# Performance work log

Hardware: AMD Instinct MI355X
Metric: run time of the kernel (lower is better)

Reference implementation:

```python
import jax, jax.numpy as jnp
import numpy as np

EPS = 1e-5
H = 6  # num_heads

def batchnorm(x, g, b):
    # BatchNorm1d over node dim using batch statistics (biased var, eps=1e-5)
    mu = x.mean(0)
    var = jnp.mean((x - mu) ** 2, 0)
    return (x - mu) * jax.lax.rsqrt(var + EPS) * g + b

def setup_inputs() -> dict:
    key = jax.random.key(0)
    ks = jax.random.split(key, 16)
    N, E, D = 20000, 200000, 384
    DH = 2 * D  # mlp hidden = dim * mlp_ratio(2.0)
    s = 0.05
    lin = lambda k, i, o: jax.random.normal(k, (i, o), jnp.float32) * s
    inp = {}
    inp['x'] = jax.random.normal(ks[0], (N, D), jnp.float32)
    inp['edge_index'] = jax.random.randint(ks[1], (2, E), 0, N)
    inp['edge_attr'] = jax.random.normal(ks[2], (E, D), jnp.float32)
    # norm1
    inp['g1'] = jnp.ones((D,), jnp.float32); inp['b1'] = jnp.zeros((D,), jnp.float32)
    # TransformerConv-style attention (concat=True, beta=False, edge_dim=D)
    inp['Wq'] = lin(ks[3], D, D); inp['bq'] = jnp.zeros((D,), jnp.float32)
    inp['Wk'] = lin(ks[4], D, D); inp['bk'] = jnp.zeros((D,), jnp.float32)
    inp['Wv'] = lin(ks[5], D, D); inp['bv'] = jnp.zeros((D,), jnp.float32)
    inp['We'] = lin(ks[6], D, D)  # lin_edge, no bias
    inp['Wskip'] = lin(ks[7], D, D); inp['bskip'] = jnp.zeros((D,), jnp.float32)
    # norm2
    inp['g2'] = jnp.ones((D,), jnp.float32); inp['b2'] = jnp.zeros((D,), jnp.float32)
    # Mlp
    inp['W1'] = lin(ks[8], D, DH); inp['bm1'] = jnp.zeros((DH,), jnp.float32)
    inp['W2'] = lin(ks[9], DH, D); inp['bm2'] = jnp.zeros((D,), jnp.float32)
    return inp

def reference(x, edge_index, edge_attr, g1, b1, Wq, bq, Wk, bk, Wv, bv, We, Wskip, bskip, g2, b2, W1, bm1, W2, bm2):
    N, D = x.shape
    Dh = D // H
    scale = 1.0 / jnp.sqrt(jnp.float32(Dh))
    h = batchnorm(x, g1, b1)
    q = (h @ Wq + bq).reshape(N, H, Dh)
    k = (h @ Wk + bk).reshape(N, H, Dh)
    v = (h @ Wv + bv).reshape(N, H, Dh)
    e = (edge_attr @ We).reshape(-1, H, Dh)  # [E,H,Dh]
    src, dst = edge_index[0], edge_index[1]
    ke = k[src] + e  # edge attr added to key
    ve = v[src] + e  # and to value (PyG TransformerConv)
    logits = jnp.einsum('ehd,ehd->eh', q[dst], ke) * scale  # [E,H]
    # segment softmax over incoming edges of each dst node
    m = jax.ops.segment_max(logits, dst, num_segments=N)
    a = jnp.exp(logits - m[dst])
    ssum = jax.ops.segment_sum(a, dst, num_segments=N)
    denom = ssum[dst]
    a = a / jnp.where(denom == 0, 1.0, denom)
    agg = jax.ops.segment_sum(a[:, :, None] * ve, dst, num_segments=N).reshape(N, D)
    attn = agg + (h @ Wskip + bskip)  # root skip (lin_skip)
    x = x + attn  # residual 1 (drop_path/dropout disabled in eval)
    h2 = batchnorm(x, g2, b2)
    mlp = jax.nn.gelu(h2 @ W1 + bm1, approximate=False) @ W2 + bm2
    return x + mlp
```

## Files before the change

### kernel.cpp

```cpp
#include <hip/hip_runtime.h>
#include <hip/hip_bf16.h>

#define DD 384
#define NH 6
#define DHID 768

typedef __attribute__((ext_vector_type(8))) short bf16x8;
typedef __attribute__((ext_vector_type(4))) float f32x4;

__device__ __forceinline__ void gload_lds16(const void* gsrc, void* ldst) {
  __builtin_amdgcn_global_load_lds((const __attribute__((address_space(1))) void*)gsrc,
                                   (__attribute__((address_space(3))) void*)ldst,
                                   16, 0, 0);
}

__device__ __forceinline__ float b2f(unsigned short u) {
  union { unsigned int i; float f; } c;
  c.i = (unsigned int)u << 16;
  return c.f;
}

__device__ __forceinline__ short f2bf(float x) {
  union { __hip_bfloat16 h; short s; } u;
  u.h = __float2bfloat16(x);
  return u.s;
}

__global__ __launch_bounds__(384) void bn_stats_k(const float* __restrict__ x, float* __restrict__ sums,
                                                  float* __restrict__ sq, int N, int rpb) {
  int d = threadIdx.x;
  int r0 = blockIdx.x * rpb;
  int r1 = min(r0 + rpb, N);
  float s = 0.f, ss = 0.f;
  for (int r = r0; r < r1; ++r) {
    float v = x[(size_t)r * DD + d];
    s += v; ss += v * v;
  }
  atomicAdd(&sums[d], s);
  atomicAdd(&sq[d], ss);
}

__global__ void bn_finalize_k(const float* sums, const float* sq, const float* g, const float* b,
                              float* a, float* c, int N) {
  int d = blockIdx.x * blockDim.x + threadIdx.x;
  if (d >= DD) return;
  float inv = 1.f / (float)N;
  float mu = sums[d] * inv;
  float var = sq[d] * inv - mu * mu;
  float rs = rsqrtf(var + 1e-5f);
  a[d] = rs * g[d];
  c[d] = b[d] - mu * rs * g[d];
}

union BPack { ushort4 u; __hip_bfloat16 b[4]; };

__global__ void norm_to_bf16_k(const float* __restrict__ x, const float* __restrict__ a,
                               const float* __restrict__ c, __hip_bfloat16* __restrict__ h, int total4) {
  int i = blockIdx.x * blockDim.x + threadIdx.x;
  if (i >= total4) return;
  float4 v = ((const float4*)x)[i];
  int d0 = (i * 4) % DD;
  float4 av = *(const float4*)(a + d0);
  float4 cv = *(const float4*)(c + d0);
  BPack p;
  p.b[0] = __float2bfloat16(v.x * av.x + cv.x);
  p.b[1] = __float2bfloat16(v.y * av.y + cv.y);
  p.b[2] = __float2bfloat16(v.z * av.z + cv.z);
  p.b[3] = __float2bfloat16(v.w * av.w + cv.w);
  ((ushort4*)h)[i] = p.u;
}

__global__ void transpose_bf16_k(const float* __restrict__ in, __hip_bfloat16* __restrict__ out,
                                 int K, int Nout) {
  int i = blockIdx.x * blockDim.x + threadIdx.x;
  if (i >= K * Nout) return;
  int k = i / Nout, n = i % Nout;
  out[(size_t)n * K + k] = __float2bfloat16(in[i]);
}

__global__ void concat_bias_k(const float* bq, const float* bk, const float* bv, const float* bs,
                              float* out) {
  int i = blockIdx.x * blockDim.x + threadIdx.x;
  if (i >= 1536) return;
  float v = (i < 384) ? bq[i] : (i < 768) ? bk[i - 384] : (i < 1152) ? bv[i - 768] : bs[i - 1152];
  out[i] = v;
}

__global__ void add3_k(const float* __restrict__ x, const float* __restrict__ agg,
                       const float* __restrict__ skip, float* __restrict__ x1, int total4) {
  int i = blockIdx.x * blockDim.x + threadIdx.x;
  if (i >= total4) return;
  float4 a = ((const float4*)x)[i];
  float4 b = ((const float4*)agg)[i];
  float4 c = ((const float4*)skip)[i];
  float4 o;
  o.x = a.x + b.x + c.x; o.y = a.y + b.y + c.y;
  o.z = a.z + b.z + c.z; o.w = a.w + b.w + c.w;
  ((float4*)x1)[i] = o;
}

__global__ void hist_k(const int* __restrict__ ei, int* __restrict__ deg, int E) {
  int i = blockIdx.x * blockDim.x + threadIdx.x;
  if (i < E) atomicAdd(&deg[ei[E + i]], 1);
}

__global__ __launch_bounds__(1024) void scan_k(const int* __restrict__ deg, int* __restrict__ row_start,
                                               int* __restrict__ cursor, int N) {
  __shared__ int part[1024];
  int t = threadIdx.x;
  int ch = (N + 1023) / 1024;
  int c0 = t * ch, c1 = min(c0 + ch, N);
  int s = 0;
  for (int i = c0; i < c1; ++i) s += deg[i];
  part[t] = s;
  __syncthreads();
  for (int off = 1; off < 1024; off <<= 1) {
    int v = (t >= off) ? part[t - off] : 0;
    __syncthreads();
    part[t] += v;
    __syncthreads();
  }
  int run = part[t] - s;
  for (int i = c0; i < c1; ++i) {
    row_start[i] = run; cursor[i] = run; run += deg[i];
  }
  if (t == 1023) row_start[N] = part[1023];
}

__global__ void scatter_k(const int* __restrict__ ei, int* __restrict__ cursor,
                          int* __restrict__ csr_src, int* __restrict__ csr_eid, int E) {
  int i = blockIdx.x * blockDim.x + threadIdx.x;
  if (i >= E) return;
  int s = ei[i], d = ei[E + i];
  int pos = atomicAdd(&cursor[d], 1);
  csr_src[pos] = s;
  csr_eid[pos] = i;
}

__global__ __launch_bounds__(256) void attn_k(const __hip_bfloat16* __restrict__ qkv,
                                              const __hip_bfloat16* __restrict__ ebuf,
                                              const int* __restrict__ row_start,
                                              const int* __restrict__ csr_src,
                                              const int* __restrict__ csr_eid,
                                              float* __restrict__ agg, int N) {
  int wid = (blockIdx.x * blockDim.x + threadIdx.x) >> 6;
  int lane = threadIdx.x & 63;
  if (wid >= N) return;
  int g = lane >> 4, l = lane & 15;
  const ushort* qk = (const ushort*)qkv;
  const ushort* eu = (const ushort*)ebuf;
  float q[NH][4], acc[NH][4], psum[NH];
#pragma unroll
  for (int h = 0; h < NH; ++h) {
    ushort4 u = *(const ushort4*)&qk[(size_t)wid * 1152 + h * 64 + l * 4];
    q[h][0] = b2f(u.x); q[h][1] = b2f(u.y); q[h][2] = b2f(u.z); q[h][3] = b2f(u.w);
#pragma unroll
    for (int j = 0; j < 4; ++j) acc[h][j] = 0.f;
    psum[h] = 0.f;
  }
  int i0 = row_start[wid], i1 = row_start[wid + 1];
  for (int i = i0; i < i1; i += 4) {
    int e = i + g;
    bool valid = e < i1;
    int ec = valid ? e : i1 - 1;
    size_t sb = (size_t)csr_src[ec] * 1152;
    size_t eb = (size_t)csr_eid[ec] * 384;
    float ev[NH][4], p[NH];
#pragma unroll
    for (int h = 0; h < NH; ++h) {
      ushort4 ue = *(const ushort4*)&eu[eb + h * 64 + l * 4];
      ev[h][0] = b2f(ue.x); ev[h][1] = b2f(ue.y); ev[h][2] = b2f(ue.z); ev[h][3] = b2f(ue.w);
      ushort4 uk = *(const ushort4*)&qk[sb + 384 + h * 64 + l * 4];
      float t = q[h][0] * (b2f(uk.x) + ev[h][0]);
      t += q[h][1] * (b2f(uk.y) + ev[h][1]);
      t += q[h][2] * (b2f(uk.z) + ev[h][2]);
      t += q[h][3] * (b2f(uk.w) + ev[h][3]);
      t += __shfl_xor(t, 1);
      t += __shfl_xor(t, 2);
      t += __shfl_xor(t, 4);
      t += __shfl_xor(t, 8);
      p[h] = valid ? __expf(t * 0.125f) : 0.f;
    }
#pragma unroll
    for (int h = 0; h < NH; ++h) {
      ushort4 uv = *(const ushort4*)&qk[sb + 768 + h * 64 + l * 4];
      acc[h][0] += p[h] * (b2f(uv.x) + ev[h][0]);
      acc[h][1] += p[h] * (b2f(uv.y) + ev[h][1]);
      acc[h][2] += p[h] * (b2f(uv.z) + ev[h][2]);
      acc[h][3] += p[h] * (b2f(uv.w) + ev[h][3]);
      psum[h] += p[h];
    }
  }
#pragma unroll
  for (int h = 0; h < NH; ++h) {
#pragma unroll
    for (int j = 0; j < 4; ++j) {
      acc[h][j] += __shfl_xor(acc[h][j], 16);
      acc[h][j] += __shfl_xor(acc[h][j], 32);
    }
    psum[h] += __shfl_xor(psum[h], 16);
    psum[h] += __shfl_xor(psum[h], 32);
  }
  if (lane < 16) {
#pragma unroll
    for (int h = 0; h < NH; ++h) {
      float inv = psum[h] > 0.f ? 1.f / psum[h] : 0.f;
      float4 o;
      o.x = acc[h][0] * inv; o.y = acc[h][1] * inv;
      o.z = acc[h][2] * inv; o.w = acc[h][3] * inv;
      *(float4*)&agg[(size_t)wid * DD + h * 64 + l * 4] = o;
    }
  }
}

#define BM 128
#define BN 128
#define BK 32

enum { M_QKVS = 0, M_BF16 = 1, M_GELU = 2, M_RES = 3 };

template <int MODE>
__global__ __launch_bounds__(256) void gemm_k(const __hip_bfloat16* __restrict__ A,
                                              const __hip_bfloat16* __restrict__ BT,
                                              const float* __restrict__ bias,
                                              const float* __restrict__ res,
                                              void* __restrict__ out0, void* __restrict__ out1,
                                              int M, int K, int Nn) {
  __shared__ short lA[2][BM * BK];
  __shared__ short lB[2][BN * BK];
  int t = threadIdx.x;
  int lane = t & 63, w = t >> 6;
  int wr = (w >> 1) * 64, wc = (w & 1) * 64;
  int row0 = blockIdx.y * BM, col0 = blockIdx.x * BN;
  int lr = lane & 15, lk = lane >> 4;
  f32x4 acc[4][4] = {};

  auto stage = [&](int b, int kt) {
#pragma unroll
    for (int j = 0; j < 2; ++j) {
      int chunk = j * 256 + t;
      int r = chunk >> 2, kc = chunk & 3;
      int wavebase = (j * 256 + w * 64) * 8;
      int gra = row0 + r; gra = gra < M ? gra : M - 1;
      gload_lds16(A + (size_t)gra * K + kt + kc * 8, &lA[b][wavebase]);
      gload_lds16(BT + (size_t)(col0 + r) * K + kt + kc * 8, &lB[b][wavebase]);
    }
  };

  stage(0, 0);
  asm volatile("s_waitcnt vmcnt(0)" ::: "memory");
  __builtin_amdgcn_s_barrier();
  int nt = K / BK, cur = 0;
  for (int ti = 0; ti < nt; ++ti) {
    if (ti + 1 < nt) stage(cur ^ 1, (ti + 1) * BK);
    bf16x8 af[4], bfr[4];
#pragma unroll
    for (int mi = 0; mi < 4; ++mi)
      af[mi] = *(const bf16x8*)&lA[cur][(wr + mi * 16 + lr) * BK + lk * 8];
#pragma unroll
    for (int ni = 0; ni < 4; ++ni)
      bfr[ni] = *(const bf16x8*)&lB[cur][(wc + ni * 16 + lr) * BK + lk * 8];
#pragma unroll
    for (int mi = 0; mi < 4; ++mi)
#pragma unroll
      for (int ni = 0; ni < 4; ++ni)
        acc[mi][ni] = __builtin_amdgcn_mfma_f32_16x16x32_bf16(af[mi], bfr[ni], acc[mi][ni], 0, 0, 0);
    asm volatile("s_waitcnt vmcnt(0)" ::: "memory");
    __builtin_amdgcn_s_barrier();
    cur ^= 1;
  }

#pragma unroll
  for (int mi = 0; mi < 4; ++mi) {
#pragma unroll
    for (int r = 0; r < 4; ++r) {
      int row = row0 + wr + mi * 16 + lk * 4 + r;
      if (row >= M) continue;
#pragma unroll
      for (int ni = 0; ni < 4; ++ni) {
        int col = col0 + wc + ni * 16 + lr;
        float v = acc[mi][ni][r];
        if constexpr (MODE == M_QKVS) {
          v += bias[col];
          if (col < 1152)
            ((__hip_bfloat16*)out0)[(size_t)row * 1152 + col] = __float2bfloat16(v);
          else
            ((float*)out1)[(size_t)row * DD + (col - 1152)] = v;
        } else if constexpr (MODE == M_BF16) {
          ((__hip_bfloat16*)out0)[(size_t)row * Nn + col] = __float2bfloat16(v);
        } else if constexpr (MODE == M_GELU) {
          v += bias[col];
          v = 0.5f * v * (1.f + erff(v * 0.70710678118f));
          ((__hip_bfloat16*)out0)[(size_t)row * Nn + col] = __float2bfloat16(v);
        } else {
          v += bias[col];
          ((float*)out0)[(size_t)row * Nn + col] = v + res[(size_t)row * Nn + col];
        }
      }
    }
  }
}

__global__ __launch_bounds__(256, 2) void gemm_edge_wide(const float* __restrict__ A,
                                                         const __hip_bfloat16* __restrict__ BT,
                                                         __hip_bfloat16* __restrict__ out, int M) {
  __shared__ float lAf[2][BM * BK];
  __shared__ short lB[2][DD * BK];
  int t = threadIdx.x;
  int lane = t & 63, w = t >> 6;
  int wr = (w >> 1) * 64, wc = (w & 1) * 192;
  int row0 = blockIdx.x * BM;
  int lr = lane & 15, lk = lane >> 4;
  f32x4 acc[4][12] = {};

  auto stage = [&](int b, int kt) {
#pragma unroll
    for (int pss = 0; pss < 6; ++pss) {
      int c = pss * 256 + t;
      int r = c >> 2, kc = c & 3;
      int wavebase = (pss * 256 + w * 64) * 8;
      gload_lds16(BT + (size_t)r * DD + kt + kc * 8, &lB[b][wavebase]);
    }
#pragma unroll
    for (int pss = 0; pss < 4; ++pss) {
      int c = pss * 256 + t;
      int r = c >> 3, slot = c & 7;
      int kc = slot ^ (r & 7);
      int gra = row0 + r; gra = gra < M ? gra : M - 1;
      int wavebase = (pss * 256 + w * 64) * 4;
      gload_lds16(A + (size_t)gra * DD + kt + kc * 4, &lAf[b][wavebase]);
    }
  };

  stage(0, 0);
  asm volatile("s_waitcnt vmcnt(0)" ::: "memory");
  __builtin_amdgcn_s_barrier();
  int nt = DD / BK, cur = 0;
  for (int ti = 0; ti < nt; ++ti) {
    if (ti + 1 < nt) stage(cur ^ 1, (ti + 1) * BK);
    bf16x8 af[4];
#pragma unroll
    for (int mi = 0; mi < 4; ++mi) {
      int r = wr + mi * 16 + lr;
      int base = r * BK;
      float4 fa = *(const float4*)&lAf[cur][base + (((2 * lk)) ^ (lr & 7)) * 4];
      float4 fb = *(const float4*)&lAf[cur][base + (((2 * lk + 1)) ^ (lr & 7)) * 4];
      bf16x8 v;
      v[0] = f2bf(fa.x); v[1] = f2bf(fa.y); v[2] = f2bf(fa.z); v[3] = f2bf(fa.w);
      v[4] = f2bf(fb.x); v[5] = f2bf(fb.y); v[6] = f2bf(fb.z); v[7] = f2bf(fb.w);
      af[mi] = v;
    }
#pragma unroll
    for (int ni = 0; ni < 12; ++ni) {
      bf16x8 bfr = *(const bf16x8*)&lB[cur][(wc + ni * 16 + lr) * BK + lk * 8];
#pragma unroll
      for (int mi = 0; mi < 4; ++mi)
        acc[mi][ni] = __builtin_amdgcn_mfma_f32_16x16x32_bf16(af[mi], bfr, acc[mi][ni], 0, 0, 0);
    }
    asm volatile("s_waitcnt vmcnt(0)" ::: "memory");
    __builtin_amdgcn_s_barrier();
    cur ^= 1;
  }

#pragma unroll
  for (int mi = 0; mi < 4; ++mi) {
#pragma unroll
    for (int r = 0; r < 4; ++r) {
      int row = row0 + wr + mi * 16 + lk * 4 + r;
      if (row >= M) continue;
#pragma unroll
      for (int ni = 0; ni < 12; ++ni) {
        int col = wc + ni * 16 + lr;
        out[(size_t)row * DD + col] = __float2bfloat16(acc[mi][ni][r]);
      }
    }
  }
}

extern "C" void kernel_launch(void* const* d_in, const int* in_sizes, int n_in,
                              void* d_out, int out_size, void* d_ws, size_t ws_size,
                              hipStream_t stream) {
  const float* x   = (const float*)d_in[0];
  const int*   ei  = (const int*)d_in[1];
  const float* ea  = (const float*)d_in[2];
  const float* g1  = (const float*)d_in[3];
  const float* b1  = (const float*)d_in[4];
  const float* Wq  = (const float*)d_in[5];
  const float* bq  = (const float*)d_in[6];
  const float* Wk  = (const float*)d_in[7];
  const float* bk  = (const float*)d_in[8];
  const float* Wv  = (const float*)d_in[9];
  const float* bv  = (const float*)d_in[10];
  const float* We  = (const float*)d_in[11];
  const float* Wsk = (const float*)d_in[12];
  const float* bsk = (const float*)d_in[13];
  const float* g2  = (const float*)d_in[14];
  const float* b2  = (const float*)d_in[15];
  const float* W1  = (const float*)d_in[16];
  const float* bm1 = (const float*)d_in[17];
  const float* W2  = (const float*)d_in[18];
  const float* bm2 = (const float*)d_in[19];

  int N = in_sizes[0] / DD;
  int E = in_sizes[1] / 2;

  char* ws = (char*)d_ws;
  size_t off = 0;
  auto alloc = [&](size_t bytes) -> char* {
    char* p = ws + off;
    off = (off + bytes + 255) & ~(size_t)255;
    return p;
  };

  float* bnsum = (float*)alloc(4 * DD * sizeof(float));
  float* a1 = (float*)alloc(DD * 4);
  float* c1 = (float*)alloc(DD * 4);
  float* a2 = (float*)alloc(DD * 4);
  float* c2 = (float*)alloc(DD * 4);
  float* bqkvs = (float*)alloc(1536 * 4);
  __hip_bfloat16* WqkvsT = (__hip_bfloat16*)alloc((size_t)1536 * DD * 2);
  __hip_bfloat16* WeT = (__hip_bfloat16*)alloc((size_t)DD * DD * 2);
  __hip_bfloat16* W1T = (__hip_bfloat16*)alloc((size_t)DHID * DD * 2);
  __hip_bfloat16* W2T = (__hip_bfloat16*)alloc((size_t)DD * DHID * 2);
  __hip_bfloat16* hbuf = (__hip_bfloat16*)alloc((size_t)N * DD * 2);
  __hip_bfloat16* qkv = (__hip_bfloat16*)alloc((size_t)N * 1152 * 2);
  float* skip = (float*)alloc((size_t)N * DD * 4);
  __hip_bfloat16* ebuf = (__hip_bfloat16*)alloc((size_t)E * DD * 2);
  float* agg = (float*)alloc((size_t)N * DD * 4);
  float* x1 = (float*)alloc((size_t)N * DD * 4);
  __hip_bfloat16* hid = (__hip_bfloat16*)alloc((size_t)N * DHID * 2);
  int* deg = (int*)alloc((size_t)N * 4);
  int* cursor = (int*)alloc((size_t)N * 4);
  int* row_start = (int*)alloc((size_t)(N + 1) * 4);
  int* csr_src = (int*)alloc((size_t)E * 4);
  int* csr_eid = (int*)alloc((size_t)E * 4);
  (void)ws_size; (void)n_in; (void)out_size;

  hipMemsetAsync(bnsum, 0, 4 * DD * sizeof(float), stream);
  hipMemsetAsync(deg, 0, (size_t)N * 4, stream);

  int rpb = 128, sgrid = (N + rpb - 1) / rpb;
  bn_stats_k<<<sgrid, DD, 0, stream>>>(x, bnsum, bnsum + DD, N, rpb);
  bn_finalize_k<<<2, 256, 0, stream>>>(bnsum, bnsum + DD, g1, b1, a1, c1, N);

  int t4 = N * DD / 4;
  norm_to_bf16_k<<<(t4 + 255) / 256, 256, 0, stream>>>(x, a1, c1, hbuf, t4);

  int wgrid = (DD * DD + 255) / 256;
  transpose_bf16_k<<<wgrid, 256, 0, stream>>>(Wq, WqkvsT, DD, DD);
  transpose_bf16_k<<<wgrid, 256, 0, stream>>>(Wk, WqkvsT + (size_t)DD * DD, DD, DD);
  transpose_bf16_k<<<wgrid, 256, 0, stream>>>(Wv, WqkvsT + (size_t)2 * DD * DD, DD, DD);
  transpose_bf16_k<<<wgrid, 256, 0, stream>>>(Wsk, WqkvsT + (size_t)3 * DD * DD, DD, DD);
  transpose_bf16_k<<<wgrid, 256, 0, stream>>>(We, WeT, DD, DD);
  transpose_bf16_k<<<(DD * DHID + 255) / 256, 256, 0, stream>>>(W1, W1T, DD, DHID);
  transpose_bf16_k<<<(DHID * DD + 255) / 256, 256, 0, stream>>>(W2, W2T, DHID, DD);
  concat_bias_k<<<6, 256, 0, stream>>>(bq, bk, bv, bsk, bqkvs);

  dim3 gqkvs(1536 / BN, (N + BM - 1) / BM);
  gemm_k<M_QKVS><<<gqkvs, 256, 0, stream>>>(hbuf, WqkvsT, bqkvs, nullptr, qkv, skip, N, DD, 1536);

  gemm_edge_wide<<<(E + BM - 1) / BM, 256, 0, stream>>>(ea, WeT, ebuf, E);

  hist_k<<<(E + 255) / 256, 256, 0, stream>>>(ei, deg, E);
  scan_k<<<1, 1024, 0, stream>>>(deg, row_start, cursor, N);
  scatter_k<<<(E + 255) / 256, 256, 0, stream>>>(ei, cursor, csr_src, csr_eid, E);

  attn_k<<<(N * 64 + 255) / 256, 256, 0, stream>>>(qkv, ebuf, row_start, csr_src, csr_eid, agg, N);

  add3_k<<<(t4 + 255) / 256, 256, 0, stream>>>(x, agg, skip, x1, t4);

  bn_stats_k<<<sgrid, DD, 0, stream>>>(x1, bnsum + 2 * DD, bnsum + 3 * DD, N, rpb);
  bn_finalize_k<<<2, 256, 0, stream>>>(bnsum + 2 * DD, bnsum + 3 * DD, g2, b2, a2, c2, N);
  norm_to_bf16_k<<<(t4 + 255) / 256, 256, 0, stream>>>(x1, a2, c2, hbuf, t4);

  dim3 gm1(DHID / BN, (N + BM - 1) / BM);
  gemm_k<M_GELU><<<gm1, 256, 0, stream>>>(hbuf, W1T, bm1, nullptr, hid, nullptr, N, DD, DHID);

  dim3 gm2(DD / BN, (N + BM - 1) / BM);
  gemm_k<M_RES><<<gm2, 256, 0, stream>>>(hid, W2T, bm2, x1, (float*)d_out, nullptr, N, DHID, DD);
}
```

Before: 597.6 us.

## Write edge projections in CSR order, parallelize scan, fuse weight prep kernels

The edge GEMM now scatters each output row to its CSR position, so the attention kernel reads edge features contiguously instead of gathering through csr_eid. CSR construction moves before the edge GEMM, and the single-block scan becomes a three-stage multi-block scan. The seven weight transposes and the bias concat are fused into one prep kernel to cut launch overhead. The cost is scattered row writes in the GEMM epilogue in exchange for sequential reads in attention.

```diff
diff --git a/kernel.cpp b/kernel.cpp
--- a/kernel.cpp
+++ b/kernel.cpp
@@ -18,12 +18,6 @@
   union { unsigned int i; float f; } c;
   c.i = (unsigned int)u << 16;
   return c.f;
-}
-
-__device__ __forceinline__ short f2bf(float x) {
-  union { __hip_bfloat16 h; short s; } u;
-  u.h = __float2bfloat16(x);
-  return u.s;
 }
 
 __global__ __launch_bounds__(384) void bn_stats_k(const float* __restrict__ x, float* __restrict__ sums,
@@ -70,20 +64,36 @@
   ((ushort4*)h)[i] = p.u;
 }
 
-__global__ void transpose_bf16_k(const float* __restrict__ in, __hip_bfloat16* __restrict__ out,
-                                 int K, int Nout) {
+__global__ void prep_k(const float* __restrict__ Wq, const float* __restrict__ Wk,
+                       const float* __restrict__ Wv, const float* __restrict__ Wsk,
+                       const float* __restrict__ We, const float* __restrict__ W1,
+                       const float* __restrict__ W2,
+                       const float* __restrict__ bq, const float* __restrict__ bk,
+                       const float* __restrict__ bv, const float* __restrict__ bsk,
+                       __hip_bfloat16* __restrict__ WqkvsT, __hip_bfloat16* __restrict__ WeT,
+                       __hip_bfloat16* __restrict__ W1T, __hip_bfloat16* __restrict__ W2T,
+                       float* __restrict__ bqkvs) {
+  const int S0 = 4 * 147456, S1 = S0 + 147456, S2 = S1 + 294912, S3 = S2 + 294912, S4 = S3 + 1536;
   int i = blockIdx.x * blockDim.x + threadIdx.x;
-  if (i >= K * Nout) return;
-  int k = i / Nout, n = i % Nout;
-  out[(size_t)n * K + k] = __float2bfloat16(in[i]);
-}
-
-__global__ void concat_bias_k(const float* bq, const float* bk, const float* bv, const float* bs,
-                              float* out) {
-  int i = blockIdx.x * blockDim.x + threadIdx.x;
-  if (i >= 1536) return;
-  float v = (i < 384) ? bq[i] : (i < 768) ? bk[i - 384] : (i < 1152) ? bv[i - 768] : bs[i - 1152];
-  out[i] = v;
+  if (i < S0) {
+    int which = i / 147456, j = i % 147456;
+    int k = j / 384, n = j % 384;
+    const float* W = which == 0 ? Wq : which == 1 ? Wk : which == 2 ? Wv : Wsk;
+    WqkvsT[(size_t)which * 147456 + n * 384 + k] = __float2bfloat16(W[j]);
+  } else if (i < S1) {
+    int j = i - S0, k = j / 384, n = j % 384;
+    WeT[(size_t)n * 384 + k] = __float2bfloat16(We[j]);
+  } else if (i < S2) {
+    int j = i - S1, k = j / 768, n = j % 768;
+    W1T[(size_t)n * 384 + k] = __float2bfloat16(W1[j]);
+  } else if (i < S3) {
+    int j = i - S2, k = j / 384, n = j % 384;
+    W2T[(size_t)n * 768 + k] = __float2bfloat16(W2[j]);
+  } else if (i < S4) {
+    int j = i - S3;
+    float v = (j < 384) ? bq[j] : (j < 768) ? bk[j - 384] : (j < 1152) ? bv[j - 768] : bsk[j - 1152];
+    bqkvs[j] = v;
+  }
 }
 
 __global__ void add3_k(const float* __restrict__ x, const float* __restrict__ agg,
@@ -104,44 +114,56 @@
   if (i < E) atomicAdd(&deg[ei[E + i]], 1);
 }
 
-__global__ __launch_bounds__(1024) void scan_k(const int* __restrict__ deg, int* __restrict__ row_start,
-                                               int* __restrict__ cursor, int N) {
-  __shared__ int part[1024];
-  int t = threadIdx.x;
-  int ch = (N + 1023) / 1024;
-  int c0 = t * ch, c1 = min(c0 + ch, N);
-  int s = 0;
-  for (int i = c0; i < c1; ++i) s += deg[i];
-  part[t] = s;
+__global__ __launch_bounds__(1024) void scan1_k(const int* __restrict__ deg, int* __restrict__ incl,
+                                                int* __restrict__ part, int N) {
+  __shared__ int sh[1024];
+  int t = threadIdx.x, i = blockIdx.x * 1024 + t;
+  int v = (i < N) ? deg[i] : 0;
+  sh[t] = v;
   __syncthreads();
   for (int off = 1; off < 1024; off <<= 1) {
-    int v = (t >= off) ? part[t - off] : 0;
+    int u = (t >= off) ? sh[t - off] : 0;
     __syncthreads();
-    part[t] += v;
+    sh[t] += u;
     __syncthreads();
   }
-  int run = part[t] - s;
-  for (int i = c0; i < c1; ++i) {
-    row_start[i] = run; cursor[i] = run; run += deg[i];
-  }
-  if (t == 1023) row_start[N] = part[1023];
+  if (i < N) incl[i] = sh[t];
+  if (t == 1023) part[blockIdx.x] = sh[1023];
+}
+
+__global__ void scan2_k(const int* __restrict__ part, int* __restrict__ partx, int nblk) {
+  if (threadIdx.x == 0 && blockIdx.x == 0) {
+    int run = 0;
+    for (int b = 0; b < nblk; ++b) { partx[b] = run; run += part[b]; }
+    partx[nblk] = run;
+  }
+}
+
+__global__ __launch_bounds__(1024) void scan3_k(const int* __restrict__ deg, const int* __restrict__ incl,
+                                                const int* __restrict__ partx, int* __restrict__ row_start,
+                                                int* __restrict__ cursor, int N, int nblk) {
+  int i = blockIdx.x * 1024 + threadIdx.x;
+  if (i >= N) return;
+  int ex = partx[blockIdx.x] + incl[i] - deg[i];
+  row_start[i] = ex;
+  cursor[i] = ex;
+  if (i == N - 1) row_start[N] = partx[nblk];
 }
 
 __global__ void scatter_k(const int* __restrict__ ei, int* __restrict__ cursor,
-                          int* __restrict__ csr_src, int* __restrict__ csr_eid, int E) {
+                          int* __restrict__ csr_src, int* __restrict__ pos_of_eid, int E) {
   int i = blockIdx.x * blockDim.x + threadIdx.x;
   if (i >= E) return;
   int s = ei[i], d = ei[E + i];
   int pos = atomicAdd(&cursor[d], 1);
   csr_src[pos] = s;
-  csr_eid[pos] = i;
+  pos_of_eid[i] = pos;
 }
 
 __global__ __launch_bounds__(256) void attn_k(const __hip_bfloat16* __restrict__ qkv,
                                               const __hip_bfloat16* __restrict__ ebuf,
                                               const int* __restrict__ row_start,
                                               const int* __restrict__ csr_src,
-                                              const int* __restrict__ csr_eid,
                                               float* __restrict__ agg, int N) {
   int wid = (blockIdx.x * blockDim.x + threadIdx.x) >> 6;
   int lane = threadIdx.x & 63;
@@ -164,7 +186,7 @@
     bool valid = e < i1;
     int ec = valid ? e : i1 - 1;
     size_t sb = (size_t)csr_src[ec] * 1152;
-    size_t eb = (size_t)csr_eid[ec] * 384;
+    size_t eb = (size_t)ec * 384;
     float ev[NH][4], p[NH];
 #pragma unroll
     for (int h = 0; h < NH; ++h) {
@@ -303,6 +325,7 @@
 
 __global__ __launch_bounds__(256, 2) void gemm_edge_wide(const float* __restrict__ A,
                                                          const __hip_bfloat16* __restrict__ BT,
+                                                         const int* __restrict__ perm,
                                                          __hip_bfloat16* __restrict__ out, int M) {
   __shared__ float lAf[2][BM * BK];
   __shared__ short lB[2][DD * BK];
@@ -346,8 +369,15 @@
       float4 fa = *(const float4*)&lAf[cur][base + (((2 * lk)) ^ (lr & 7)) * 4];
       float4 fb = *(const float4*)&lAf[cur][base + (((2 * lk + 1)) ^ (lr & 7)) * 4];
       bf16x8 v;
-      v[0] = f2bf(fa.x); v[1] = f2bf(fa.y); v[2] = f2bf(fa.z); v[3] = f2bf(fa.w);
-      v[4] = f2bf(fb.x); v[5] = f2bf(fb.y); v[6] = f2bf(fb.z); v[7] = f2bf(fb.w);
+      union { __hip_bfloat16 h; short s; } u;
+      u.h = __float2bfloat16(fa.x); v[0] = u.s;
+      u.h = __float2bfloat16(fa.y); v[1] = u.s;
+      u.h = __float2bfloat16(fa.z); v[2] = u.s;
+      u.h = __float2bfloat16(fa.w); v[3] = u.s;
+      u.h = __float2bfloat16(fb.x); v[4] = u.s;
+      u.h = __float2bfloat16(fb.y); v[5] = u.s;
+      u.h = __float2bfloat16(fb.z); v[6] = u.s;
+      u.h = __float2bfloat16(fb.w); v[7] = u.s;
       af[mi] = v;
     }
 #pragma unroll
@@ -368,10 +398,11 @@
     for (int r = 0; r < 4; ++r) {
       int row = row0 + wr + mi * 16 + lk * 4 + r;
       if (row >= M) continue;
+      size_t orow = (size_t)perm[row];
 #pragma unroll
       for (int ni = 0; ni < 12; ++ni) {
         int col = wc + ni * 16 + lr;
-        out[(size_t)row * DD + col] = __float2bfloat16(acc[mi][ni][r]);
+        out[orow * DD + col] = __float2bfloat16(acc[mi][ni][r]);
       }
     }
   }
@@ -433,11 +464,21 @@
   int* cursor = (int*)alloc((size_t)N * 4);
   int* row_start = (int*)alloc((size_t)(N + 1) * 4);
   int* csr_src = (int*)alloc((size_t)E * 4);
-  int* csr_eid = (int*)alloc((size_t)E * 4);
+  int* pos_of_eid = (int*)alloc((size_t)E * 4);
+  int* incl = (int*)alloc((size_t)N * 4);
+  int* part = (int*)alloc(64 * 4);
+  int* partx = (int*)alloc(64 * 4);
   (void)ws_size; (void)n_in; (void)out_size;
 
   hipMemsetAsync(bnsum, 0, 4 * DD * sizeof(float), stream);
   hipMemsetAsync(deg, 0, (size_t)N * 4, stream);
+
+  int nblk = (N + 1023) / 1024;
+  hist_k<<<(E + 255) / 256, 256, 0, stream>>>(ei, deg, E);
+  scan1_k<<<nblk, 1024, 0, stream>>>(deg, incl, part, N);
+  scan2_k<<<1, 64, 0, stream>>>(part, partx, nblk);
+  scan3_k<<<nblk, 1024, 0, stream>>>(deg, incl, partx, row_start, cursor, N, nblk);
+  scatter_k<<<(E + 255) / 256, 256, 0, stream>>>(ei, cursor, csr_src, pos_of_eid, E);
 
   int rpb = 128, sgrid = (N + rpb - 1) / rpb;
   bn_stats_k<<<sgrid, DD, 0, stream>>>(x, bnsum, bnsum + DD, N, rpb);
@@ -446,26 +487,17 @@
   int t4 = N * DD / 4;
   norm_to_bf16_k<<<(t4 + 255) / 256, 256, 0, stream>>>(x, a1, c1, hbuf, t4);
 
-  int wgrid = (DD * DD + 255) / 256;
-  transpose_bf16_k<<<wgrid, 256, 0, stream>>>(Wq, WqkvsT, DD, DD);
-  transpose_bf16_k<<<wgrid, 256, 0, stream>>>(Wk, WqkvsT + (size_t)DD * DD, DD, DD);
-  transpose_bf16_k<<<wgrid, 256, 0, stream>>>(Wv, WqkvsT + (size_t)2 * DD * DD, DD, DD);
-  transpose_bf16_k<<<wgrid, 256, 0, stream>>>(Wsk, WqkvsT + (size_t)3 * DD * DD, DD, DD);
-  transpose_bf16_k<<<wgrid, 256, 0, stream>>>(We, WeT, DD, DD);
-  transpose_bf16_k<<<(DD * DHID + 255) / 256, 256, 0, stream>>>(W1, W1T, DD, DHID);
-  transpose_bf16_k<<<(DHID * DD + 255) / 256, 256, 0, stream>>>(W2, W2T, DHID, DD);
-  concat_bias_k<<<6, 256, 0, stream>>>(bq, bk, bv, bsk, bqkvs);
+  const int PREP_TOT = 4 * 147456 + 147456 + 294912 + 294912 + 1536;
+  prep_k<<<(PREP_TOT + 255) / 256, 256, 0, stream>>>(Wq, Wk, Wv, Wsk, We, W1, W2,
+                                                     bq, bk, bv, bsk,
+                                                     WqkvsT, WeT, W1T, W2T, bqkvs);
 
   dim3 gqkvs(1536 / BN, (N + BM - 1) / BM);
   gemm_k<M_QKVS><<<gqkvs, 256, 0, stream>>>(hbuf, WqkvsT, bqkvs, nullptr, qkv, skip, N, DD, 1536);
 
-  gemm_edge_wide<<<(E + BM - 1) / BM, 256, 0, stream>>>(ea, WeT, ebuf, E);
-
-  hist_k<<<(E + 255) / 256, 256, 0, stream>>>(ei, deg, E);
-  scan_k<<<1, 1024, 0, stream>>>(deg, row_start, cursor, N);
-  scatter_k<<<(E + 255) / 256, 256, 0, stream>>>(ei, cursor, csr_src, csr_eid, E);
-
-  attn_k<<<(N * 64 + 255) / 256, 256, 0, stream>>>(qkv, ebuf, row_start, csr_src, csr_eid, agg, N);
+  gemm_edge_wide<<<(E + BM - 1) / BM, 256, 0, stream>>>(ea, WeT, pos_of_eid, ebuf, E);
+
+  attn_k<<<(N * 64 + 255) / 256, 256, 0, stream>>>(qkv, ebuf, row_start, csr_src, agg, N);
 
   add3_k<<<(t4 + 255) / 256, 256, 0, stream>>>(x, agg, skip, x1, t4);
 
```

Measured after the change: 562.2 us, median of 3. -5.9%, faster.
